# Optimization experiments

Hardware: AMD Instinct MI355X
Metric: run time of the kernel (lower is better)

## Reference

```python
import jax, jax.numpy as jnp
import numpy as np

B, N, T, D = 4, 8, 4096, 1024  # batch, n_concepts, tokens, d_model
TEMPERATURE = 1.0


def setup_inputs() -> dict:
    key = jax.random.key(0)
    k1, k2 = jax.random.split(key)
    e_aggregated = jax.random.normal(k1, (B, N, T, D), dtype=jnp.float32)
    scaler_weight = jax.random.normal(k2, (N, D, 1), dtype=jnp.float32)
    return {"e_aggregated": e_aggregated, "scaler_weight": scaler_weight}


def reference(e_aggregated, scaler_weight):
    n_concepts = scaler_weight.shape[0]
    # scores: [b, n, t, 1] via einsum 'ndi,bntd->bnti'
    scale = jax.nn.sigmoid(TEMPERATURE * jnp.einsum('ndi,bntd->bnti', scaler_weight, e_aggregated))
    scale_max_val = jnp.max(scale, axis=1, keepdims=True)      # [b,1,t,1]
    scale_max_ind = jnp.argmax(scale, axis=1, keepdims=True)   # [b,1,t,1]
    # one_hot(squeeze(-1)) -> [b,1,t,n]; permute(0,3,2,1) -> [b,n,t,1]
    one_hot_f = jax.nn.one_hot(scale_max_ind[..., 0], n_concepts, dtype=e_aggregated.dtype)
    ind_one_hot = jnp.transpose(one_hot_f, (0, 3, 2, 1))        # [b,n,t,1]
    # masked combine: select winning concept, weight by its gate value
    e_out = jnp.sum(scale_max_val * ind_one_hot * e_aggregated, axis=1)  # [b,t,d]
    return (e_out, ind_one_hot.astype(jnp.int32), scale_max_val, scale_max_ind.astype(jnp.int32))
```

## Files before the change

### kernel.cpp

```cpp
#include <hip/hip_runtime.h>
#include <math.h>

#define BB 4
#define NN 8
#define TT 4096
#define DD 1024

__global__ __launch_bounds__(256) void gate_kernel(
    const float* __restrict__ e,
    const float* __restrict__ w,
    float* __restrict__ e_out,
    float* __restrict__ one_hot,
    float* __restrict__ smax,
    float* __restrict__ sind)
{
    const int lane = threadIdx.x & 63;
    const int wid  = blockIdx.x * 4 + (threadIdx.x >> 6);
    const int b    = wid >> 12;
    const int t    = wid & (TT - 1);

    const int dl = lane * 4;

    float dot[NN];
#pragma unroll
    for (int n = 0; n < NN; ++n) dot[n] = 0.0f;

#pragma unroll
    for (int n = 0; n < NN; ++n) {
        const float* ep = e + (((size_t)b * NN + n) * TT + t) * DD + dl;
        const float* wp = w + (size_t)n * DD + dl;
#pragma unroll
        for (int r = 0; r < 4; ++r) {
            const float4 ef = *reinterpret_cast<const float4*>(ep + r * 256);
            const float4 wf = *reinterpret_cast<const float4*>(wp + r * 256);
            dot[n] += ef.x * wf.x + ef.y * wf.y + ef.z * wf.z + ef.w * wf.w;
        }
    }

#pragma unroll
    for (int off = 32; off > 0; off >>= 1) {
#pragma unroll
        for (int n = 0; n < NN; ++n)
            dot[n] += __shfl_xor(dot[n], off, 64);
    }

    float best = -1.0f;
    int   bi   = 0;
#pragma unroll
    for (int n = 0; n < NN; ++n) {
        const float sn = 1.0f / (1.0f + expf(-dot[n]));
        if (sn > best) { best = sn; bi = n; }
    }

    if (lane == 0) {
        smax[wid] = best;
        sind[wid] = (float)bi;
    }
    if (lane < NN) {
        one_hot[((size_t)b * NN + lane) * TT + t] = (lane == bi) ? 1.0f : 0.0f;
    }

    const float* wr = e + (((size_t)b * NN + bi) * TT + t) * DD + dl;
    float*       op = e_out + ((size_t)b * TT + t) * DD + dl;
#pragma unroll
    for (int r = 0; r < 4; ++r) {
        float4 o = *reinterpret_cast<const float4*>(wr + r * 256);
        o.x *= best; o.y *= best; o.z *= best; o.w *= best;
        *reinterpret_cast<float4*>(op + r * 256) = o;
    }
}

extern "C" void kernel_launch(void* const* d_in, const int* in_sizes, int n_in,
                              void* d_out, int out_size, void* d_ws, size_t ws_size,
                              hipStream_t stream) {
    const float* e = (const float*)d_in[0];
    const float* w = (const float*)d_in[1];

    float* out     = (float*)d_out;
    float* e_out   = out;
    float* one_hot = e_out + (size_t)BB * TT * DD;
    float* smax    = one_hot + (size_t)BB * NN * TT;
    float* sind    = smax + (size_t)BB * TT;

    gate_kernel<<<(BB * TT) / 4, 256, 0, stream>>>(e, w, e_out, one_hot, smax, sind);
}
```

Measured before the change: 122.6 us.

## Keep winning concept rows in registers to avoid re-reading input, process two tokens per wave

After: 100.3 us. 1.22x faster.

```diff
diff --git a/kernel.cpp b/kernel.cpp
--- a/kernel.cpp
+++ b/kernel.cpp
@@ -5,6 +5,8 @@
 #define NN 8
 #define TT 4096
 #define DD 1024
+
+typedef float vfloat4 __attribute__((ext_vector_type(4)));
 
 __global__ __launch_bounds__(256) void gate_kernel(
     const float* __restrict__ e,
@@ -14,60 +16,92 @@
     float* __restrict__ smax,
     float* __restrict__ sind)
 {
-    const int lane = threadIdx.x & 63;
-    const int wid  = blockIdx.x * 4 + (threadIdx.x >> 6);
-    const int b    = wid >> 12;
-    const int t    = wid & (TT - 1);
+    const int lane  = threadIdx.x & 63;
+    const int wpair = blockIdx.x * 4 + (threadIdx.x >> 6);
+    const int wid0  = wpair * 2;
+    const int b     = wid0 >> 12;
+    const int t0    = wid0 & (TT - 1);
+    const int dl    = lane * 4;
 
-    const int dl = lane * 4;
-
-    float dot[NN];
-#pragma unroll
-    for (int n = 0; n < NN; ++n) dot[n] = 0.0f;
+    float   bsA = -1.0f, bsB = -1.0f;
+    int     biA = 0,     biB = 0;
+    vfloat4 a0, a1, a2, a3;
+    vfloat4 e0, e1, e2, e3;
 
 #pragma unroll
     for (int n = 0; n < NN; ++n) {
-        const float* ep = e + (((size_t)b * NN + n) * TT + t) * DD + dl;
-        const float* wp = w + (size_t)n * DD + dl;
+        const float* epA = e + (((size_t)b * NN + n) * TT + t0) * DD + dl;
+        const float* epB = epA + DD;
+        const float* wp  = w + (size_t)n * DD + dl;
+
+        const vfloat4 cA0 = __builtin_nontemporal_load(reinterpret_cast<const vfloat4*>(epA));
+        const vfloat4 cA1 = __builtin_nontemporal_load(reinterpret_cast<const vfloat4*>(epA + 256));
+        const vfloat4 cA2 = __builtin_nontemporal_load(reinterpret_cast<const vfloat4*>(epA + 512));
+        const vfloat4 cA3 = __builtin_nontemporal_load(reinterpret_cast<const vfloat4*>(epA + 768));
+        const vfloat4 cB0 = __builtin_nontemporal_load(reinterpret_cast<const vfloat4*>(epB));
+        const vfloat4 cB1 = __builtin_nontemporal_load(reinterpret_cast<const vfloat4*>(epB + 256));
+        const vfloat4 cB2 = __builtin_nontemporal_load(reinterpret_cast<const vfloat4*>(epB + 512));
+        const vfloat4 cB3 = __builtin_nontemporal_load(reinterpret_cast<const vfloat4*>(epB + 768));
+        const vfloat4 w0  = *reinterpret_cast<const vfloat4*>(wp);
+        const vfloat4 w1  = *reinterpret_cast<const vfloat4*>(wp + 256);
+        const vfloat4 w2  = *reinterpret_cast<const vfloat4*>(wp + 512);
+        const vfloat4 w3  = *reinterpret_cast<const vfloat4*>(wp + 768);
+
+        float dA = cA0.x * w0.x + cA0.y * w0.y + cA0.z * w0.z + cA0.w * w0.w;
+        dA      += cA1.x * w1.x + cA1.y * w1.y + cA1.z * w1.z + cA1.w * w1.w;
+        dA      += cA2.x * w2.x + cA2.y * w2.y + cA2.z * w2.z + cA2.w * w2.w;
+        dA      += cA3.x * w3.x + cA3.y * w3.y + cA3.z * w3.z + cA3.w * w3.w;
+        float dB = cB0.x * w0.x + cB0.y * w0.y + cB0.z * w0.z + cB0.w * w0.w;
+        dB      += cB1.x * w1.x + cB1.y * w1.y + cB1.z * w1.z + cB1.w * w1.w;
+        dB      += cB2.x * w2.x + cB2.y * w2.y + cB2.z * w2.z + cB2.w * w2.w;
+        dB      += cB3.x * w3.x + cB3.y * w3.y + cB3.z * w3.z + cB3.w * w3.w;
+
 #pragma unroll
-        for (int r = 0; r < 4; ++r) {
-            const float4 ef = *reinterpret_cast<const float4*>(ep + r * 256);
-            const float4 wf = *reinterpret_cast<const float4*>(wp + r * 256);
-            dot[n] += ef.x * wf.x + ef.y * wf.y + ef.z * wf.z + ef.w * wf.w;
+        for (int off = 32; off > 0; off >>= 1) {
+            dA += __shfl_xor(dA, off, 64);
+            dB += __shfl_xor(dB, off, 64);
+        }
+
+        const float sA = 1.0f / (1.0f + expf(-dA));
+        const float sB = 1.0f / (1.0f + expf(-dB));
+
+        if (n == 0) {
+            bsA = sA; biA = 0; a0 = cA0; a1 = cA1; a2 = cA2; a3 = cA3;
+            bsB = sB; biB = 0; e0 = cB0; e1 = cB1; e2 = cB2; e3 = cB3;
+        } else {
+            const bool tkA = (sA > bsA);
+            if (tkA) { bsA = sA; biA = n; }
+            a0 = tkA ? cA0 : a0;  a1 = tkA ? cA1 : a1;
+            a2 = tkA ? cA2 : a2;  a3 = tkA ? cA3 : a3;
+            const bool tkB = (sB > bsB);
+            if (tkB) { bsB = sB; biB = n; }
+            e0 = tkB ? cB0 : e0;  e1 = tkB ? cB1 : e1;
+            e2 = tkB ? cB2 : e2;  e3 = tkB ? cB3 : e3;
         }
     }
 
-#pragma unroll
-    for (int off = 32; off > 0; off >>= 1) {
-#pragma unroll
-        for (int n = 0; n < NN; ++n)
-            dot[n] += __shfl_xor(dot[n], off, 64);
+    if (lane == 0) {
+        smax[wid0]     = bsA;  sind[wid0]     = (float)biA;
+        smax[wid0 + 1] = bsB;  sind[wid0 + 1] = (float)biB;
+    }
+    if (lane < NN) {
+        const size_t oh = ((size_t)b * NN + lane) * TT + t0;
+        one_hot[oh]     = (lane == biA) ? 1.0f : 0.0f;
+        one_hot[oh + 1] = (lane == biB) ? 1.0f : 0.0f;
     }
 
-    float best = -1.0f;
-    int   bi   = 0;
-#pragma unroll
-    for (int n = 0; n < NN; ++n) {
-        const float sn = 1.0f / (1.0f + expf(-dot[n]));
-        if (sn > best) { best = sn; bi = n; }
-    }
-
-    if (lane == 0) {
-        smax[wid] = best;
-        sind[wid] = (float)bi;
-    }
-    if (lane < NN) {
-        one_hot[((size_t)b * NN + lane) * TT + t] = (lane == bi) ? 1.0f : 0.0f;
-    }
-
-    const float* wr = e + (((size_t)b * NN + bi) * TT + t) * DD + dl;
-    float*       op = e_out + ((size_t)b * TT + t) * DD + dl;
-#pragma unroll
-    for (int r = 0; r < 4; ++r) {
-        float4 o = *reinterpret_cast<const float4*>(wr + r * 256);
-        o.x *= best; o.y *= best; o.z *= best; o.w *= best;
-        *reinterpret_cast<float4*>(op + r * 256) = o;
-    }
+    float* opA = e_out + ((size_t)b * TT + t0) * DD + dl;
+    float* opB = opA + DD;
+    a0 *= bsA; a1 *= bsA; a2 *= bsA; a3 *= bsA;
+    e0 *= bsB; e1 *= bsB; e2 *= bsB; e3 *= bsB;
+    __builtin_nontemporal_store(a0, reinterpret_cast<vfloat4*>(opA));
+    __builtin_nontemporal_store(a1, reinterpret_cast<vfloat4*>(opA + 256));
+    __builtin_nontemporal_store(a2, reinterpret_cast<vfloat4*>(opA + 512));
+    __builtin_nontemporal_store(a3, reinterpret_cast<vfloat4*>(opA + 768));
+    __builtin_nontemporal_store(e0, reinterpret_cast<vfloat4*>(opB));
+    __builtin_nontemporal_store(e1, reinterpret_cast<vfloat4*>(opB + 256));
+    __builtin_nontemporal_store(e2, reinterpret_cast<vfloat4*>(opB + 512));
+    __builtin_nontemporal_store(e3, reinterpret_cast<vfloat4*>(opB + 768));
 }
 
 extern "C" void kernel_launch(void* const* d_in, const int* in_sizes, int n_in,
@@ -82,5 +116,5 @@
     float* smax    = one_hot + (size_t)BB * NN * TT;
     float* sind    = smax + (size_t)BB * TT;
 
-    gate_kernel<<<(BB * TT) / 4, 256, 0, stream>>>(e, w, e_out, one_hot, smax, sind);
+    gate_kernel<<<(BB * TT) / 8, 256, 0, stream>>>(e, w, e_out, one_hot, smax, sind);
 }
```
